# Optimization experiments

Hardware: AMD Instinct MI355X
Metric: run time of the kernel (lower is better)

Reference implementation:

```python
import jax, jax.numpy as jnp
import numpy as np

C_IN = 128
D_K = 256
D_V = 256
N_HEAD = 8
H = 192
W = 192
REGION = 3
TEMPER = int(np.sqrt(D_K))  # int(sqrt(d_k)) per the torch module


def setup_inputs() -> dict:
    key = jax.random.key(0)
    k1, k2, k3, k4 = jax.random.split(key, 4)
    scale = 1.0 / np.sqrt(C_IN).astype(np.float32)
    x = jax.random.normal(k1, (1, C_IN, H, W), dtype=jnp.float32)
    wq = jax.random.normal(k2, (D_K, C_IN), dtype=jnp.float32) * scale
    wk = jax.random.normal(k3, (D_K, C_IN), dtype=jnp.float32) * scale
    wv = jax.random.normal(k4, (D_V, C_IN), dtype=jnp.float32) * scale
    return {"x": x, "wq": wq, "wk": wk, "wv": wv}


def _stretch(t):
    # Equivalent of the fixed Conv3d 'stretch' trick: for each (i, j) in the
    # 3x3 region, channel 3*i+j holds the input shifted by (i-1, j-1), zero-padded.
    # t: [b, d, H, W] -> [b, 9, d, H, W]
    b, d, h, w = t.shape
    tp = jnp.pad(t, ((0, 0), (0, 0), (1, 1), (1, 1)))
    return jnp.stack(
        [tp[:, :, i:i + h, j:j + w] for i in range(REGION) for j in range(REGION)],
        axis=1,
    )


def reference(x, wq, wk, wv):
    b = x.shape[0]  # must be 1 (module's broadcast only works for batch 1)
    dkh = D_K // N_HEAD
    dvh = D_V // N_HEAD
    r2 = REGION * REGION
    # 1x1 conv projections == channel matmuls
    q = jnp.einsum('oc,bchw->bohw', wq, x)
    k = jnp.einsum('oc,bchw->bohw', wk, x)
    v = jnp.einsum('oc,bchw->bohw', wv, x)
    Q = _stretch(q)  # [b, 9, d_k, H, W]
    K = _stretch(k)
    V = _stretch(v)  # [b, 9, d_v, H, W]
    # elementwise QK, per-head channel sum, scale, softmax over the 9 region slots
    qk = (Q * K).reshape(b, r2, N_HEAD, dkh, H, W)
    scores = jax.nn.softmax(qk.sum(axis=3) / TEMPER, axis=1)  # [b, 9, n_head, H, W]
    # dropout is identity in eval mode (att_drop disabled for the reference)
    Vh = V.reshape(b, r2, N_HEAD, dvh, H, W)
    out = (scores[:, :, :, None] * Vh).sum(axis=1).reshape(b, D_V, H, W)
    return out
```

## Files before the change

### kernel.cpp

```cpp
#include <hip/hip_runtime.h>

#define HW_   36864
#define WI    192
#define HT    192
#define CIN   128
#define DK    256
#define NH    8
#define DKH   32

using short8  = __attribute__((ext_vector_type(8))) short;
using float4_ = __attribute__((ext_vector_type(4))) float;

static __device__ __forceinline__ float b2f(unsigned short u) {
    union { unsigned int i; float f; } x; x.i = ((unsigned int)u) << 16; return x.f;
}
static __device__ __forceinline__ unsigned short f2b(float f) {
    union { float f; unsigned int i; } x; x.f = f;
    unsigned int r = x.i + 0x7FFFu + ((x.i >> 16) & 1u);
    return (unsigned short)(r >> 16);
}

__global__ __launch_bounds__(256) void detect_kernel(
    const unsigned int* __restrict__ xw, int* __restrict__ flag)
{
    __shared__ int sh[256];
    int t = threadIdx.x;
    int cnt = 0;
    for (int i = t; i < 4096; i += 256) {
        unsigned int w = xw[i];
        unsigned int e = (w >> 23) & 0xFF;
        if (e >= 96 && e <= 160) cnt++;
    }
    sh[t] = cnt;
    __syncthreads();
    for (int s = 128; s > 0; s >>= 1) {
        if (t < s) sh[t] += sh[t + s];
        __syncthreads();
    }
    if (t == 0) *flag = (sh[0] > 2048) ? 1 : 0;
}

__global__ __launch_bounds__(256) void convw_kernel(
    const void* __restrict__ wq,
    const void* __restrict__ wk,
    const void* __restrict__ wv,
    const int* __restrict__ flag,
    unsigned short* __restrict__ wqkv)
{
    int id = blockIdx.x * 256 + threadIdx.x;
    int h   = id / 12288;
    int rem = id - h * 12288;
    int r   = rem >> 7;
    int c   = rem & 127;
    const void* s = (r < 32) ? wq : ((r < 64) ? wk : wv);
    int si = (h * 32 + (r & 31)) * 128 + c;
    if (*flag) wqkv[id] = f2b(((const float*)s)[si]);
    else       wqkv[id] = ((const unsigned short*)s)[si];
}

__global__ __launch_bounds__(256) void convx_kernel(
    const void* __restrict__ x, const int* __restrict__ flag,
    unsigned short* __restrict__ xt)
{
    __shared__ unsigned short tile[64][136];
    const int px0 = blockIdx.x * 64;
    const int t = threadIdx.x;
    if (*flag) {
        const float* __restrict__ xf = (const float*)x;
        for (int i = 0; i < 32; ++i) {
            int id = i * 256 + t;
            int c = id >> 6, p = id & 63;
            tile[p][c] = f2b(xf[c * HW_ + px0 + p]);
        }
    } else {
        const unsigned short* __restrict__ xb = (const unsigned short*)x;
        for (int i = 0; i < 32; ++i) {
            int id = i * 256 + t;
            int c = id >> 6, p = id & 63;
            tile[p][c] = xb[c * HW_ + px0 + p];
        }
    }
    __syncthreads();
    for (int i = 0; i < 4; ++i) {
        int id = i * 256 + t;
        int row = id >> 4, c8 = id & 15;
        *(short8*)&xt[(px0 + row) * 128 + c8 * 8] =
            *(const short8*)&tile[row][c8 * 8];
    }
}

__global__ __launch_bounds__(256) void projmm_kernel(
    const unsigned short* __restrict__ xt,
    const unsigned short* __restrict__ wqkv,
    unsigned short* __restrict__ vbuf,
    float* __restrict__ sbuf)
{
    __shared__ unsigned short As[96 * 136];
    __shared__ unsigned short Bs[128 * 136];
    const int head = blockIdx.x;
    const int px0  = blockIdx.y * 128;
    const int t = threadIdx.x;

    const unsigned short* __restrict__ Ag = wqkv + head * 96 * 128;
    #pragma unroll
    for (int i = 0; i < 6; ++i) {
        int id = i * 256 + t;
        int row = id >> 4, c8 = id & 15;
        *(short8*)&As[row * 136 + c8 * 8] = *(const short8*)&Ag[row * 128 + c8 * 8];
    }
    const unsigned short* __restrict__ Bg = xt + px0 * 128;
    #pragma unroll
    for (int i = 0; i < 8; ++i) {
        int id = i * 256 + t;
        int row = id >> 4, c8 = id & 15;
        *(short8*)&Bs[row * 136 + c8 * 8] = *(const short8*)&Bg[row * 128 + c8 * 8];
    }
    __syncthreads();

    const int lane = t & 63, wave = t >> 6;
    const int col = lane & 15, quad = lane >> 4;

    short8 bfrag[2][4];
    #pragma unroll
    for (int nt = 0; nt < 2; ++nt)
        #pragma unroll
        for (int kt = 0; kt < 4; ++kt) {
            int n = wave * 32 + nt * 16 + col;
            bfrag[nt][kt] = *(const short8*)&Bs[n * 136 + kt * 32 + quad * 8];
        }

    float4_ acc[6][2];
    #pragma unroll
    for (int mt = 0; mt < 6; ++mt)
        #pragma unroll
        for (int nt = 0; nt < 2; ++nt)
            acc[mt][nt] = (float4_){0.f, 0.f, 0.f, 0.f};

    #pragma unroll
    for (int mt = 0; mt < 6; ++mt) {
        #pragma unroll
        for (int kt = 0; kt < 4; ++kt) {
            int m = mt * 16 + col;
            short8 a = *(const short8*)&As[m * 136 + kt * 32 + quad * 8];
            acc[mt][0] = __builtin_amdgcn_mfma_f32_16x16x32_bf16(a, bfrag[0][kt], acc[mt][0], 0, 0, 0);
            acc[mt][1] = __builtin_amdgcn_mfma_f32_16x16x32_bf16(a, bfrag[1][kt], acc[mt][1], 0, 0, 0);
        }
    }

    #pragma unroll
    for (int nt = 0; nt < 2; ++nt) {
        int px = px0 + wave * 32 + nt * 16 + col;
        float s = 0.f;
        #pragma unroll
        for (int reg = 0; reg < 4; ++reg)
            s += acc[0][nt][reg] * acc[2][nt][reg]
               + acc[1][nt][reg] * acc[3][nt][reg];
        s += __shfl_xor(s, 16, 64);
        s += __shfl_xor(s, 32, 64);
        if (quad == 0) sbuf[head * HW_ + px] = s;
        #pragma unroll
        for (int mt = 4; mt < 6; ++mt)
            #pragma unroll
            for (int reg = 0; reg < 4; ++reg) {
                int d = head * 32 + (mt - 4) * 16 + quad * 4 + reg;
                vbuf[d * HW_ + px] = f2b(acc[mt][nt][reg]);
            }
    }
}

__global__ __launch_bounds__(256) void attn_kernel(
    const unsigned short* __restrict__ vbuf,
    const float* __restrict__ sbuf,
    const int* __restrict__ flag,
    void* __restrict__ out)
{
    const int b    = blockIdx.x;
    const int head = b / 144;
    const int px   = (b % 144) * 256 + threadIdx.x;
    const int y    = px / WI;
    const int xx   = px - y * WI;
    const bool f32 = (*flag != 0);

    const float* __restrict__ Sh = sbuf + head * HW_;

    float w[9];
    int   np[9];
    float m = -1e30f;
    #pragma unroll
    for (int r = 0; r < 9; ++r) {
        int dy = r / 3 - 1, dx = r % 3 - 1;
        int ny = y + dy, nx = xx + dx;
        bool inb = (ny >= 0) && (ny < HT) && (nx >= 0) && (nx < WI);
        int idx = inb ? (ny * WI + nx) : px;
        np[r] = idx;
        float val = inb ? (Sh[idx] * 0.0625f) : 0.0f;
        w[r] = val;
        m = fmaxf(m, val);
    }
    float wsum = 0.f;
    #pragma unroll
    for (int r = 0; r < 9; ++r) {
        float e = __expf(w[r] - m);
        w[r] = e;
        wsum += e;
    }
    float inv = 1.0f / wsum;
    #pragma unroll
    for (int r = 0; r < 9; ++r) {
        int dy = r / 3 - 1, dx = r % 3 - 1;
        int ny = y + dy, nx = xx + dx;
        bool inb = (ny >= 0) && (ny < HT) && (nx >= 0) && (nx < WI);
        w[r] = inb ? (w[r] * inv) : 0.0f;
    }

    const unsigned short* __restrict__ vb = vbuf + head * DKH * HW_;
    const int obase = head * DKH * HW_;
    for (int ch = 0; ch < DKH; ++ch) {
        const unsigned short* __restrict__ vc = vb + ch * HW_;
        float acc = 0.f;
        #pragma unroll
        for (int r = 0; r < 9; ++r)
            acc = fmaf(w[r], b2f(vc[np[r]]), acc);
        int oi = obase + ch * HW_ + px;
        if (f32) ((float*)out)[oi] = acc;
        else     ((unsigned short*)out)[oi] = f2b(acc);
    }
}

extern "C" void kernel_launch(void* const* d_in, const int* in_sizes, int n_in,
                              void* d_out, int out_size, void* d_ws, size_t ws_size,
                              hipStream_t stream) {
    const void* x  = d_in[0];
    const void* wq = d_in[1];
    const void* wk = d_in[2];
    const void* wv = d_in[3];

    char* ws = (char*)d_ws;
    int*            flag = (int*)ws;
    unsigned short* wqkv = (unsigned short*)(ws + 256);
    unsigned short* xt   = (unsigned short*)(ws + 196864);
    unsigned short* vbuf = (unsigned short*)(ws + 9634048);
    float*          sbuf = (float*)(ws + 28508416);

    detect_kernel<<<1, 256, 0, stream>>>((const unsigned int*)x, flag);
    convw_kernel<<<384, 256, 0, stream>>>(wq, wk, wv, flag, wqkv);
    convx_kernel<<<576, 256, 0, stream>>>(x, flag, xt);
    projmm_kernel<<<dim3(8, 288), 256, 0, stream>>>(xt, wqkv, vbuf, sbuf);
    attn_kernel<<<1152, 256, 0, stream>>>(vbuf, sbuf, flag, (void*)d_out);
}
```

Measured before the change: 125.8 us.

## Store V pixel-major per head and vectorize attention gathers via LDS transpose

The projection kernel now writes V as [head][pixel][32 channels], so each pixel's head slice is contiguous and written with 8-byte vector stores instead of scattered 2-byte stores across channel planes. The attention kernel splits each pixel across 4 threads, each gathering 8 channels per neighbour with a 16-byte load. It then transposes through shared memory so output stays channel-major with coalesced vector stores. This costs extra LDS traffic, a barrier and 4x more blocks, in exchange for far fewer scattered global accesses.

Result: faster. 120.3 us (-4.4%).

```diff
diff --git a/kernel.cpp b/kernel.cpp
--- a/kernel.cpp
+++ b/kernel.cpp
@@ -8,6 +8,7 @@
 #define NH    8
 #define DKH   32
 
+using short4_ = __attribute__((ext_vector_type(4))) short;
 using short8  = __attribute__((ext_vector_type(8))) short;
 using float4_ = __attribute__((ext_vector_type(4))) float;
 
@@ -158,13 +159,15 @@
         s += __shfl_xor(s, 16, 64);
         s += __shfl_xor(s, 32, 64);
         if (quad == 0) sbuf[head * HW_ + px] = s;
-        #pragma unroll
-        for (int mt = 4; mt < 6; ++mt)
-            #pragma unroll
-            for (int reg = 0; reg < 4; ++reg) {
-                int d = head * 32 + (mt - 4) * 16 + quad * 4 + reg;
-                vbuf[d * HW_ + px] = f2b(acc[mt][nt][reg]);
-            }
+        unsigned short* vp = vbuf + ((size_t)head * HW_ + px) * 32;
+        short4_ v0, v1;
+        #pragma unroll
+        for (int reg = 0; reg < 4; ++reg) {
+            v0[reg] = (short)f2b(acc[4][nt][reg]);
+            v1[reg] = (short)f2b(acc[5][nt][reg]);
+        }
+        *(short4_*)&vp[quad * 4]      = v0;
+        *(short4_*)&vp[16 + quad * 4] = v1;
     }
 }
 
@@ -174,9 +177,14 @@
     const int* __restrict__ flag,
     void* __restrict__ out)
 {
+    __shared__ float tr[32][65];
     const int b    = blockIdx.x;
-    const int head = b / 144;
-    const int px   = (b % 144) * 256 + threadIdx.x;
+    const int tile = b % 576;
+    const int head = b / 576;
+    const int t    = threadIdx.x;
+    const int pxl  = t >> 2;
+    const int cg   = t & 3;
+    const int px   = tile * 64 + pxl;
     const int y    = px / WI;
     const int xx   = px - y * WI;
     const bool f32 = (*flag != 0);
@@ -213,17 +221,39 @@
         w[r] = inb ? (w[r] * inv) : 0.0f;
     }
 
-    const unsigned short* __restrict__ vb = vbuf + head * DKH * HW_;
-    const int obase = head * DKH * HW_;
-    for (int ch = 0; ch < DKH; ++ch) {
-        const unsigned short* __restrict__ vc = vb + ch * HW_;
-        float acc = 0.f;
-        #pragma unroll
-        for (int r = 0; r < 9; ++r)
-            acc = fmaf(w[r], b2f(vc[np[r]]), acc);
-        int oi = obase + ch * HW_ + px;
-        if (f32) ((float*)out)[oi] = acc;
-        else     ((unsigned short*)out)[oi] = f2b(acc);
+    const unsigned short* __restrict__ vb = vbuf + (size_t)head * HW_ * 32;
+    float acc[8] = {0.f, 0.f, 0.f, 0.f, 0.f, 0.f, 0.f, 0.f};
+    #pragma unroll
+    for (int r = 0; r < 9; ++r) {
+        short8 v8 = *(const short8*)&vb[np[r] * 32 + cg * 8];
+        #pragma unroll
+        for (int j = 0; j < 8; ++j)
+            acc[j] = fmaf(w[r], b2f((unsigned short)v8[j]), acc[j]);
+    }
+    #pragma unroll
+    for (int j = 0; j < 8; ++j)
+        tr[cg * 8 + j][pxl] = acc[j];
+    __syncthreads();
+
+    const int ch = t >> 3, c8 = t & 7;
+    const int px0 = tile * 64;
+    const size_t obase = (size_t)(head * DKH + ch) * HW_ + px0 + c8 * 8;
+    if (f32) {
+        float4_ o0, o1;
+        #pragma unroll
+        for (int j = 0; j < 4; ++j) {
+            o0[j] = tr[ch][c8 * 8 + j];
+            o1[j] = tr[ch][c8 * 8 + 4 + j];
+        }
+        float* o = (float*)out + obase;
+        *(float4_*)&o[0] = o0;
+        *(float4_*)&o[4] = o1;
+    } else {
+        short8 o8;
+        #pragma unroll
+        for (int j = 0; j < 8; ++j)
+            o8[j] = (short)f2b(tr[ch][c8 * 8 + j]);
+        *(short8*)((unsigned short*)out + obase) = o8;
     }
 }
 
@@ -246,5 +276,5 @@
     convw_kernel<<<384, 256, 0, stream>>>(wq, wk, wv, flag, wqkv);
     convx_kernel<<<576, 256, 0, stream>>>(x, flag, xt);
     projmm_kernel<<<dim3(8, 288), 256, 0, stream>>>(xt, wqkv, vbuf, sbuf);
-    attn_kernel<<<1152, 256, 0, stream>>>(vbuf, sbuf, flag, (void*)d_out);
-}
+    attn_kernel<<<4608, 256, 0, stream>>>(vbuf, sbuf, flag, (void*)d_out);
+}
```
